# Performance work log

Measured on AMD Instinct MI355X. Metric: run time of the kernel, lower is better.

## Reference

```python
import jax, jax.numpy as jnp
import numpy as np

DIM = 1024
NUM_HEADS = 16
HEAD_DIM = DIM // NUM_HEADS
SEQ = 2048
BATCH = 2


def setup_inputs() -> dict:
    key = jax.random.key(0)
    kx, kq, kk, kv, ko, kb = jax.random.split(key, 6)
    s = 0.02
    return {
        "x": jax.random.normal(kx, (BATCH, SEQ, DIM), dtype=jnp.float32),
        "W_q": jax.random.normal(kq, (DIM, DIM), dtype=jnp.float32) * s,
        "W_k": jax.random.normal(kk, (DIM, DIM), dtype=jnp.float32) * s,
        "W_v": jax.random.normal(kv, (DIM, DIM), dtype=jnp.float32) * s,
        "W_o": jax.random.normal(ko, (DIM, DIM), dtype=jnp.float32) * s,
        "b_o": jax.random.normal(kb, (DIM,), dtype=jnp.float32) * s,
    }


def reference(x, W_q, W_k, W_v, W_o, b_o):
    b, n, d = x.shape
    # Linear layers (torch Linear: y = x @ W.T); weights here stored as [out, in]
    q = jnp.einsum('bnd,ed->bne', x, W_q).reshape(b, n, NUM_HEADS, HEAD_DIM)
    k = jnp.einsum('bnd,ed->bne', x, W_k).reshape(b, n, NUM_HEADS, HEAD_DIM)
    v = jnp.einsum('bnd,ed->bne', x, W_v).reshape(b, n, NUM_HEADS, HEAD_DIM)
    # scores: [b, h, q, k]
    scores = jnp.einsum('bqhd,bkhd->bhqk', q, k)
    causal = jnp.tril(jnp.ones((n, n), dtype=bool))  # True = keep
    scores = jnp.where(causal, scores, -jnp.inf)
    weights = jax.nn.softmax(scores / jnp.sqrt(jnp.float32(HEAD_DIM)), axis=-1)
    ctx = jnp.einsum('bhqk,bkhd->bqhd', weights, v).reshape(b, n, d)
    return jnp.einsum('bnd,ed->bne', ctx, W_o) + b_o
```

## Files before the change

### kernel.cpp

```cpp
#include <hip/hip_runtime.h>
#include <hip/hip_bf16.h>

#define DIM 1024
#define NHEADS 16
#define HD 64
#define SEQ 2048
#define BATCH 2
#define MROWS (BATCH * SEQ)
#define MB (1024u * 1024u)
#define NT (SEQ / 64)

typedef __bf16 bf16x8 __attribute__((ext_vector_type(8)));
typedef float f32x4 __attribute__((ext_vector_type(4)));
typedef short short8 __attribute__((ext_vector_type(8)));

#define SCQ (0.125f * 1.44269504f)

__device__ __forceinline__ unsigned short f2bf(float f) {
    union { float f; unsigned u; } v; v.f = f;
    unsigned r = v.u + 0x7fffu + ((v.u >> 16) & 1u);
    return (unsigned short)(r >> 16);
}
__device__ __forceinline__ unsigned cvtpk(float lo, float hi) {
    unsigned r;
    asm("v_cvt_pk_bf16_f32 %0, %1, %2" : "=v"(r) : "v"(lo), "v"(hi));
    return r;
}

__device__ __forceinline__ void gld16(const unsigned short* g, unsigned short* l) {
    __builtin_amdgcn_global_load_lds(
        (const __attribute__((address_space(1))) void*)g,
        (__attribute__((address_space(3))) void*)l, 16, 0, 0);
}

#define VWAIT(n) asm volatile("s_waitcnt vmcnt(" #n ")" ::: "memory")
#define BARRIER  do { __builtin_amdgcn_s_barrier(); __builtin_amdgcn_sched_barrier(0); } while (0)

__global__ __launch_bounds__(256) void f2all_kernel(
    const float* __restrict__ x,
    const float* __restrict__ w0, const float* __restrict__ w1,
    const float* __restrict__ w2, const float* __restrict__ w3,
    unsigned short* __restrict__ xb,
    unsigned short* __restrict__ o0, unsigned short* __restrict__ o1,
    unsigned short* __restrict__ o2, unsigned short* __restrict__ o3)
{
    const float* in; unsigned short* out; int n4;
    switch (blockIdx.y) {
        case 0: in = x;  out = xb; n4 = (MROWS * DIM) / 4; break;
        case 1: in = w0; out = o0; n4 = (DIM * DIM) / 4;   break;
        case 2: in = w1; out = o1; n4 = (DIM * DIM) / 4;   break;
        case 3: in = w2; out = o2; n4 = (DIM * DIM) / 4;   break;
        default: in = w3; out = o3; n4 = (DIM * DIM) / 4;  break;
    }
    int i = blockIdx.x * 256 + threadIdx.x;
    if (i < n4) {
        float4 v = ((const float4*)in)[i];
        ushort4 o;
        o.x = f2bf(v.x); o.y = f2bf(v.y); o.z = f2bf(v.z); o.w = f2bf(v.w);
        ((ushort4*)out)[i] = o;
    }
}


#define GEMM_VARS(Aptr, Bptr)                                                  \
    __shared__ unsigned short As[3][128 * 32];                                 \
    __shared__ unsigned short Bs[3][128 * 32];                                 \
    const int tid  = threadIdx.x;                                              \
    const int lane = tid & 63;                                                 \
    const int wid  = tid >> 6;                                                 \
    const int wrow = wid >> 1, wcol = wid & 1;                                 \
    const int l15  = lane & 15;                                                \
    const int lhi  = lane >> 4;                                                \
    f32x4 acc[4][4] = {};                                                      \
    const int r0s = tid >> 2;                                                  \
    const int c0s = (tid & 3) ^ ((r0s >> 1) & 3);                              \
    const int r1s = (tid + 256) >> 2;                                          \
    const int c1s = (tid & 3) ^ ((r1s >> 1) & 3);                              \
    const unsigned short* gA0 = (Aptr) + (size_t)(row0 + r0s) * DIM + c0s * 8; \
    const unsigned short* gA1 = (Aptr) + (size_t)(row0 + r1s) * DIM + c1s * 8; \
    const unsigned short* gB0 = (Bptr) + (size_t)(col0 + r0s) * DIM + c0s * 8; \
    const unsigned short* gB1 = (Bptr) + (size_t)(col0 + r1s) * DIM + c1s * 8;

#define GEMM_STAGE(bi, kofs)                                                   \
    gld16(gA0 + (kofs), &As[bi][tid * 8]);                                     \
    gld16(gA1 + (kofs), &As[bi][(tid + 256) * 8]);                             \
    gld16(gB0 + (kofs), &Bs[bi][tid * 8]);                                     \
    gld16(gB1 + (kofs), &Bs[bi][(tid + 256) * 8]);

#define GEMM_COMPUTE(bi)                                                       \
    {   const unsigned short* Ac = &As[bi][0];                                 \
        const unsigned short* Bc = &Bs[bi][0];                                 \
        bf16x8 af[4], bfr[4];                                                  \
        _Pragma("unroll")                                                      \
        for (int m = 0; m < 4; m++) {                                          \
            int r = wrow * 64 + m * 16 + l15;                                  \
            int c = lhi ^ ((r >> 1) & 3);                                      \
            af[m] = *(const bf16x8*)&Ac[r * 32 + c * 8];                       \
        }                                                                      \
        _Pragma("unroll")                                                      \
        for (int n = 0; n < 4; n++) {                                          \
            int r = wcol * 64 + n * 16 + l15;                                  \
            int c = lhi ^ ((r >> 1) & 3);                                      \
            bfr[n] = *(const bf16x8*)&Bc[r * 32 + c * 8];                      \
        }                                                                      \
        __builtin_amdgcn_s_setprio(1);                                         \
        _Pragma("unroll")                                                      \
        for (int m = 0; m < 4; m++)                                            \
            _Pragma("unroll")                                                  \
            for (int n = 0; n < 4; n++)                                        \
                acc[m][n] = __builtin_amdgcn_mfma_f32_16x16x32_bf16(           \
                    af[m], bfr[n], acc[m][n], 0, 0, 0);                        \
        __builtin_amdgcn_s_setprio(0);                                         \
    }

#define GEMM_PIPELINE()                                                        \
    GEMM_STAGE(0, 0)                                                           \
    GEMM_STAGE(1, 32)                                                          \
    int bi = 0;                                                                \
    for (int k0 = 0; k0 + 96 <= DIM; k0 += 32) {                               \
        VWAIT(4);                                                              \
        BARRIER;                                                               \
        int b2 = bi + 2; if (b2 >= 3) b2 -= 3;                                 \
        GEMM_STAGE(b2, k0 + 64)                                                \
        GEMM_COMPUTE(bi)                                                       \
        bi = (bi + 1 == 3) ? 0 : bi + 1;                                       \
    }                                                                          \
    VWAIT(4);                                                                  \
    BARRIER;                                                                   \
    GEMM_COMPUTE(bi)                                                           \
    bi = (bi + 1 == 3) ? 0 : bi + 1;                                           \
    VWAIT(0);                                                                  \
    BARRIER;                                                                   \
    GEMM_COMPUTE(bi)

__global__ __launch_bounds__(256) void qkv_gemm(
    const unsigned short* __restrict__ A,
    const unsigned short* __restrict__ Wqb,
    const unsigned short* __restrict__ Wkb,
    const unsigned short* __restrict__ Wvb,
    unsigned short* __restrict__ Qb,
    unsigned short* __restrict__ Kbf,
    unsigned short* __restrict__ Vtb)
{
    const int lb  = ((int)blockIdx.x & 7) * 96 + ((int)blockIdx.x >> 3);
    const int xx  = lb % 24;
    const int yy  = lb / 24;
    const int sel = xx >> 3;
    const unsigned short* Bw = (sel == 0) ? Wqb : ((sel == 1) ? Wkb : Wvb);
    const int row0 = yy * 128;
    const int col0 = (xx & 7) * 128;

    GEMM_VARS(A, Bw)
    GEMM_PIPELINE()

    const int cr = lhi * 4;
    unsigned short* outRM = (sel == 0) ? Qb : Kbf;
    #pragma unroll
    for (int m = 0; m < 4; m++) {
        #pragma unroll
        for (int n = 0; n < 4; n++) {
            #pragma unroll
            for (int j = 0; j < 4; j++) {
                int gr = row0 + wrow * 64 + m * 16 + cr + j;
                int gc = col0 + wcol * 64 + n * 16 + l15;
                float v = acc[m][n][j];
                if (sel == 0) v *= SCQ;
                unsigned short hv = f2bf(v);
                if (sel < 2) {
                    outRM[(size_t)gr * DIM + gc] = hv;
                } else {
                    int bb = gr >> 11, s = gr & 2047;
                    int hh = gc >> 6,  d = gc & 63;
                    Vtb[(((size_t)bb * NHEADS + hh) * HD + d) * SEQ + s] = hv;
                }
            }
        }
    }
}

__global__ __launch_bounds__(256) void o_gemm(
    const unsigned short* __restrict__ A,
    const unsigned short* __restrict__ Bw,
    float* __restrict__ Cp,
    const float* __restrict__ bias)
{
    const int lb  = ((int)blockIdx.x & 7) * 32 + ((int)blockIdx.x >> 3);
    const int xx  = lb % 8;
    const int yy  = lb / 8;
    const int row0 = yy * 128;
    const int col0 = xx * 128;

    GEMM_VARS(A, Bw)
    GEMM_PIPELINE()

    const int cr = lhi * 4;
    #pragma unroll
    for (int m = 0; m < 4; m++) {
        #pragma unroll
        for (int n = 0; n < 4; n++) {
            #pragma unroll
            for (int j = 0; j < 4; j++) {
                int gr = row0 + wrow * 64 + m * 16 + cr + j;
                int gc = col0 + wcol * 64 + n * 16 + l15;
                Cp[(size_t)gr * DIM + gc] = acc[m][n][j] + bias[gc];
            }
        }
    }
}

#define ATTN_COMPUTE(bi, t)                                                    \
    {   const unsigned short* Kc = &Ks[bi][0];                                 \
        const unsigned short* Vc = &Vs[bi][0];                                 \
        f32x4 sacc[4] = {};                                                    \
        __builtin_amdgcn_s_setprio(1);                                         \
        _Pragma("unroll")                                                      \
        for (int ks = 0; ks < 2; ++ks) {                                       \
            bf16x8 bq = ks ? aq1 : aq0;                                        \
            _Pragma("unroll")                                                  \
            for (int nt = 0; nt < 4; nt++) {                                   \
                int r = nt * 16 + l15;                                         \
                int c = (ks * 4 + lhi) ^ (r & 7);                              \
                bf16x8 ak = *(const bf16x8*)&Kc[r * 64 + c * 8];               \
                sacc[nt] = __builtin_amdgcn_mfma_f32_16x16x32_bf16(            \
                    ak, bq, sacc[nt], 0, 0, 0);                                \
            }                                                                  \
        }                                                                      \
        __builtin_amdgcn_s_setprio(0);                                         \
        const bool diag = ((t) == qblk);                                       \
        _Pragma("unroll")                                                      \
        for (int nt = 0; nt < 4; nt++) {                                       \
            float pv[4];                                                       \
            _Pragma("unroll")                                                  \
            for (int j = 0; j < 4; j++) {                                      \
                bool msk = diag && (nt * 16 + lhi * 4 + j > (w & 3) * 16 + l15); \
                pv[j] = msk ? 0.f : exp2f(sacc[nt][j]);                        \
            }                                                                  \
            *(uint2*)&Ps[w][l15][nt * 16 + lhi * 4] =                          \
                make_uint2(cvtpk(pv[0], pv[1]), cvtpk(pv[2], pv[3]));          \
        }                                                                      \
        __builtin_amdgcn_s_setprio(1);                                         \
        _Pragma("unroll")                                                      \
        for (int ks = 0; ks < 2; ++ks) {                                       \
            bf16x8 ap = *(const bf16x8*)&Ps[w][l15][ks * 32 + lhi * 8];        \
            _Pragma("unroll")                                                  \
            for (int dt = 0; dt < 4; dt++) {                                   \
                int r = dt * 16 + l15;                                         \
                int c = (ks * 4 + lhi) ^ (r & 7);                              \
                bf16x8 bv = *(const bf16x8*)&Vc[r * 64 + c * 8];               \
                octx[dt] = __builtin_amdgcn_mfma_f32_16x16x32_bf16(            \
                    ap, bv, octx[dt], 0, 0, 0);                                \
            }                                                                  \
            octxS = __builtin_amdgcn_mfma_f32_16x16x32_bf16(ap, vones, octxS, 0, 0, 0); \
        }                                                                      \
        __builtin_amdgcn_s_setprio(0);                                         \
    }

__global__ __launch_bounds__(512) void attn_kernel(
    const unsigned short* __restrict__ Q,
    const unsigned short* __restrict__ Kb,
    const unsigned short* __restrict__ Vt,
    unsigned short* __restrict__ Ctx)
{
    __shared__ unsigned short Ks[3][64 * 64];
    __shared__ unsigned short Vs[3][64 * 64];
    __shared__ unsigned short Ps[8][16][72];

    const int tid  = threadIdx.x;
    const int lane = tid & 63;
    const int w    = tid >> 6;
    const int bid  = (int)blockIdx.x;
    const int half = bid >> 8;
    const int idx  = bid & 255;
    const int h    = idx & 15;
    const int b    = (idx >> 4) & 1;
    const int slot = idx >> 5;
    const int p    = half ? slot : (15 - slot);
    const int l15  = lane & 15;
    const int lhi  = lane >> 4;

    const int qblk   = 2 * p + (w >> 2);
    const int qw     = qblk * 64 + (w & 3) * 16;
    const int ntiles = 2 * p + 2;

    const size_t qrow = ((size_t)b * SEQ + qw + l15) * DIM + h * HD;
    bf16x8 aq0 = *(const bf16x8*)(Q + qrow + lhi * 8);
    bf16x8 aq1 = *(const bf16x8*)(Q + qrow + 32 + lhi * 8);

    const int srow = tid >> 3;
    const int sc16 = (tid & 7) ^ (srow & 7);
    const unsigned short* gK = Kb + ((size_t)b * SEQ + srow) * DIM + h * HD + sc16 * 8;
    const unsigned short* gV = Vt + (((size_t)b * NHEADS + h) * HD + srow) * SEQ + sc16 * 8;

    bf16x8 vones;
    #pragma unroll
    for (int i = 0; i < 8; i++) vones[i] = (__bf16)1.0f;

    f32x4 octx[4] = {};
    f32x4 octxS = {};

    gld16(gK,                    &Ks[0][tid * 8]);
    gld16(gV,                    &Vs[0][tid * 8]);
    gld16(gK + (size_t)64 * DIM, &Ks[1][tid * 8]);
    gld16(gV + 64,               &Vs[1][tid * 8]);

    int bi = 0;
    for (int t = 0; t < ntiles; ++t) {
        if (t < ntiles - 1) { VWAIT(2); } else { VWAIT(0); }
        BARRIER;
        if (t + 2 < ntiles) {
            int b2 = bi + 2; if (b2 >= 3) b2 -= 3;
            gld16(gK + (size_t)(t + 2) * 64 * DIM, &Ks[b2][tid * 8]);
            gld16(gV + (size_t)(t + 2) * 64,       &Vs[b2][tid * 8]);
        }
        if (t <= qblk) ATTN_COMPUTE(bi, t);
        bi = (bi + 1 == 3) ? 0 : bi + 1;
    }

    #pragma unroll
    for (int j = 0; j < 4; j++) {
        float inv = 1.0f / octxS[j];
        #pragma unroll
        for (int dt = 0; dt < 4; dt++) {
            Ctx[((size_t)b * SEQ + qw + lhi * 4 + j) * DIM + h * HD + dt * 16 + l15] =
                f2bf(octx[dt][j] * inv);
        }
    }
}

extern "C" void kernel_launch(void* const* d_in, const int* in_sizes, int n_in,
                              void* d_out, int out_size, void* d_ws, size_t ws_size,
                              hipStream_t stream) {
    const float* x  = (const float*)d_in[0];
    const float* Wq = (const float*)d_in[1];
    const float* Wk = (const float*)d_in[2];
    const float* Wv = (const float*)d_in[3];
    const float* Wo = (const float*)d_in[4];
    const float* bo = (const float*)d_in[5];

    char* ws = (char*)d_ws;
    unsigned short* xb   = (unsigned short*)(ws + 0 * MB);
    unsigned short* Wqb  = (unsigned short*)(ws + 8 * MB);
    unsigned short* Wkb  = (unsigned short*)(ws + 10 * MB);
    unsigned short* Wvb  = (unsigned short*)(ws + 12 * MB);
    unsigned short* Wob  = (unsigned short*)(ws + 14 * MB);
    unsigned short* Qb   = (unsigned short*)(ws + 16 * MB);
    unsigned short* Kbf  = (unsigned short*)(ws + 24 * MB);
    unsigned short* Vtb  = (unsigned short*)(ws + 32 * MB);
    unsigned short* ctxb = (unsigned short*)(ws + 40 * MB);

    f2all_kernel<<<dim3(4096, 5), 256, 0, stream>>>(x, Wq, Wk, Wv, Wo,
                                                    xb, Wqb, Wkb, Wvb, Wob);

    qkv_gemm<<<768, 256, 0, stream>>>(xb, Wqb, Wkb, Wvb, Qb, Kbf, Vtb);

    attn_kernel<<<512, 512, 0, stream>>>(Qb, Kbf, Vtb, ctxb);

    o_gemm<<<256, 256, 0, stream>>>(ctxb, Wob, (float*)d_out, bo);
}
```

Measured before the change: 122.7 us.

## Load GEMM B operand directly from global into registers, dropping LDS staging

The B (weight) tile is no longer staged through the shared-memory triple buffer. Each warp now reads its B fragments straight from global memory into registers at every k-step, while A keeps its asynchronous global-to-LDS pipeline. This halves LDS footprint and traffic and removes the B swizzle reads. In exchange, the B loads are issued just before the MFMAs with no prefetch, so global latency may be exposed each iteration, and warps sharing a column re-read the same weights.

```diff
diff --git a/kernel.cpp b/kernel.cpp
--- a/kernel.cpp
+++ b/kernel.cpp
@@ -35,6 +35,7 @@
 
 #define VWAIT(n) asm volatile("s_waitcnt vmcnt(" #n ")" ::: "memory")
 #define BARRIER  do { __builtin_amdgcn_s_barrier(); __builtin_amdgcn_sched_barrier(0); } while (0)
+#define SBAR     __builtin_amdgcn_sched_barrier(0)
 
 __global__ __launch_bounds__(256) void f2all_kernel(
     const float* __restrict__ x,
@@ -64,7 +65,6 @@
 
 #define GEMM_VARS(Aptr, Bptr)                                                  \
     __shared__ unsigned short As[3][128 * 32];                                 \
-    __shared__ unsigned short Bs[3][128 * 32];                                 \
     const int tid  = threadIdx.x;                                              \
     const int lane = tid & 63;                                                 \
     const int wid  = tid >> 6;                                                 \
@@ -78,30 +78,33 @@
     const int c1s = (tid & 3) ^ ((r1s >> 1) & 3);                              \
     const unsigned short* gA0 = (Aptr) + (size_t)(row0 + r0s) * DIM + c0s * 8; \
     const unsigned short* gA1 = (Aptr) + (size_t)(row0 + r1s) * DIM + c1s * 8; \
-    const unsigned short* gB0 = (Bptr) + (size_t)(col0 + r0s) * DIM + c0s * 8; \
-    const unsigned short* gB1 = (Bptr) + (size_t)(col0 + r1s) * DIM + c1s * 8;
+    const unsigned short* gBF = (Bptr) + (size_t)(col0 + wcol * 64 + l15) * DIM + lhi * 8;
 
 #define GEMM_STAGE(bi, kofs)                                                   \
     gld16(gA0 + (kofs), &As[bi][tid * 8]);                                     \
-    gld16(gA1 + (kofs), &As[bi][(tid + 256) * 8]);                             \
-    gld16(gB0 + (kofs), &Bs[bi][tid * 8]);                                     \
-    gld16(gB1 + (kofs), &Bs[bi][(tid + 256) * 8]);
-
-#define GEMM_COMPUTE(bi)                                                       \
-    {   const unsigned short* Ac = &As[bi][0];                                 \
-        const unsigned short* Bc = &Bs[bi][0];                                 \
-        bf16x8 af[4], bfr[4];                                                  \
+    gld16(gA1 + (kofs), &As[bi][(tid + 256) * 8]);
+
+#define GEMM_ITER(t, bi)                                                       \
+    {                                                                          \
+        if ((t) < 30) { VWAIT(2); } else { VWAIT(0); }                         \
+        BARRIER;                                                               \
+        bf16x8 bfr[4];                                                         \
+        _Pragma("unroll")                                                      \
+        for (int n = 0; n < 4; n++)                                            \
+            bfr[n] = *(const bf16x8*)(gBF + (size_t)(n * 16) * DIM + (t) * 32);\
+        SBAR;                                                                  \
+        if ((t) + 2 < 32) {                                                    \
+            int b2 = (bi) + 2; if (b2 >= 3) b2 -= 3;                           \
+            GEMM_STAGE(b2, ((t) + 2) * 32)                                     \
+        }                                                                      \
+        SBAR;                                                                  \
+        const unsigned short* Ac = &As[bi][0];                                 \
+        bf16x8 af[4];                                                          \
         _Pragma("unroll")                                                      \
         for (int m = 0; m < 4; m++) {                                          \
             int r = wrow * 64 + m * 16 + l15;                                  \
             int c = lhi ^ ((r >> 1) & 3);                                      \
             af[m] = *(const bf16x8*)&Ac[r * 32 + c * 8];                       \
-        }                                                                      \
-        _Pragma("unroll")                                                      \
-        for (int n = 0; n < 4; n++) {                                          \
-            int r = wcol * 64 + n * 16 + l15;                                  \
-            int c = lhi ^ ((r >> 1) & 3);                                      \
-            bfr[n] = *(const bf16x8*)&Bc[r * 32 + c * 8];                      \
         }                                                                      \
         __builtin_amdgcn_s_setprio(1);                                         \
         _Pragma("unroll")                                                      \
@@ -117,21 +120,10 @@
     GEMM_STAGE(0, 0)                                                           \
     GEMM_STAGE(1, 32)                                                          \
     int bi = 0;                                                                \
-    for (int k0 = 0; k0 + 96 <= DIM; k0 += 32) {                               \
-        VWAIT(4);                                                              \
-        BARRIER;                                                               \
-        int b2 = bi + 2; if (b2 >= 3) b2 -= 3;                                 \
-        GEMM_STAGE(b2, k0 + 64)                                                \
-        GEMM_COMPUTE(bi)                                                       \
+    for (int t = 0; t < 32; ++t) {                                             \
+        GEMM_ITER(t, bi)                                                       \
         bi = (bi + 1 == 3) ? 0 : bi + 1;                                       \
-    }                                                                          \
-    VWAIT(4);                                                                  \
-    BARRIER;                                                                   \
-    GEMM_COMPUTE(bi)                                                           \
-    bi = (bi + 1 == 3) ? 0 : bi + 1;                                           \
-    VWAIT(0);                                                                  \
-    BARRIER;                                                                   \
-    GEMM_COMPUTE(bi)
+    }
 
 __global__ __launch_bounds__(256) void qkv_gemm(
     const unsigned short* __restrict__ A,
```

After: 155.9 us. 27.0% more time.
